# Kernel optimization log

Measured on AMD Instinct MI355X. Metric: run time of the kernel, lower is better.

## Reference

```python
import jax, jax.numpy as jnp
import numpy as np

NUM_NETS = 262144
PINS_PER_NET = 4
NUM_PINS = NUM_NETS * PINS_PER_NET
NBX, NBY = 256, 256
XL, XH, YL, YH = 0.0, 512.0, 0.0, 512.0
BSX = (XH - XL) / NBX
BSY = (YH - YL) / NBY

# RISA wiring-distribution weight table, indexed by pin count (clamped at 46).
_RISA_TAB = jnp.asarray(np.array(
    [1.0, 1.0, 1.0, 1.0,
     1.0828, 1.1536, 1.2206, 1.2823, 1.3385, 1.3991, 1.4493]
    + [1.6899] * 5 + [1.8924] * 5 + [2.0743] * 5 + [2.2334] * 5
    + [2.3892] * 5 + [2.5356] * 5 + [2.6625] * 5 + [2.7933],
    dtype=np.float32))


def setup_inputs() -> dict:
    key = jax.random.key(0)
    k1, k2 = jax.random.split(key)
    # pin positions, interleaved xyxy..., uniform inside the layout region
    pin_pos = jax.random.uniform(k1, (2 * NUM_PINS,), jnp.float32, XL, XH)
    # CSR offsets: 4 pins per net (ragged structure handled generically below)
    netpin_start = jnp.arange(NUM_NETS + 1, dtype=jnp.int32) * PINS_PER_NET
    # flat net->pin map: a permutation of all pin ids
    flat_netpin = jax.random.permutation(k2, jnp.arange(NUM_PINS, dtype=jnp.int32))
    net_weights = jnp.ones((NUM_NETS,), jnp.float32)
    return {"pin_pos": pin_pos, "netpin_start": netpin_start,
            "flat_netpin": flat_netpin, "net_weights": net_weights}


def _net_density(pin_pos, netpin_start, flat_netpin, net_weights):
    num_nets = netpin_start.shape[0] - 1
    num_pins = flat_netpin.shape[0]
    # pin i (in flat order) belongs to net n with netpin_start[n] <= i < netpin_start[n+1]
    pin2net = jnp.searchsorted(netpin_start,
                               jnp.arange(num_pins, dtype=netpin_start.dtype),
                               side='right') - 1
    px = pin_pos[2 * flat_netpin]
    py = pin_pos[2 * flat_netpin + 1]
    # per-net bounding boxes via segment max/min
    x_max = jax.ops.segment_max(px, pin2net, num_segments=num_nets)
    x_min = -jax.ops.segment_max(-px, pin2net, num_segments=num_nets)
    y_max = jax.ops.segment_max(py, pin2net, num_segments=num_nets)
    y_min = -jax.ops.segment_max(-py, pin2net, num_segments=num_nets)
    # RISA weight from pin count, times the net weight
    cnt = netpin_start[1:] - netpin_start[:-1]
    wt = _RISA_TAB[jnp.minimum(cnt, _RISA_TAB.shape[0] - 1)] * net_weights
    # per-bin overlap lengths (separable in x and y): [num_nets, NBX] / [num_nets, NBY]
    bxl = XL + BSX * jnp.arange(NBX, dtype=pin_pos.dtype)
    byl = YL + BSY * jnp.arange(NBY, dtype=pin_pos.dtype)
    ox = jnp.clip(jnp.minimum(x_max[:, None], bxl + BSX) - jnp.maximum(x_min[:, None], bxl), 0.0)
    oy = jnp.clip(jnp.minimum(y_max[:, None], byl + BSY) - jnp.maximum(y_min[:, None], byl), 0.0)
    dx = x_max - x_min
    dy = y_max - y_min
    # horizontal demand ~ wt/dy, vertical demand ~ wt/dx (guard degenerate bboxes)
    ch = jnp.where(dy > 0, wt / jnp.maximum(dy, 1e-12), 0.0)
    cv = jnp.where(dx > 0, wt / jnp.maximum(dx, 1e-12), 0.0)
    # scatter-add over bins expressed as a dense contraction over nets
    H = jnp.einsum('nx,ny->xy', ch[:, None] * ox, oy)
    V = jnp.einsum('nx,ny->xy', cv[:, None] * ox, oy)
    return jnp.abs(H) + jnp.abs(V), H, V


def reference(pin_pos, netpin_start, flat_netpin, net_weights):
    return _net_density(pin_pos, netpin_start, flat_netpin, net_weights)
```

## Files before the change

kernel.cpp:

```cpp
#include <hip/hip_runtime.h>


#define NBX 256
#define NBY 256
#define CELLS (NBX * NBY)
#define STRIPS 16
#define SROWS 16
#define HALF_TILE (SROWS * NBY)
#define TILE_FLOATS (HALF_TILE * 2)
#define NSCAT 512
#define TOTAL_ENT 724992

#define BS_ 2.0f
#define INV_BS 0.5f

__constant__ float c_risa[47] = {
    1.0f, 1.0f, 1.0f, 1.0f,
    1.0828f, 1.1536f, 1.2206f, 1.2823f, 1.3385f, 1.3991f, 1.4493f,
    1.6899f, 1.6899f, 1.6899f, 1.6899f, 1.6899f,
    1.8924f, 1.8924f, 1.8924f, 1.8924f, 1.8924f,
    2.0743f, 2.0743f, 2.0743f, 2.0743f, 2.0743f,
    2.2334f, 2.2334f, 2.2334f, 2.2334f, 2.2334f,
    2.3892f, 2.3892f, 2.3892f, 2.3892f, 2.3892f,
    2.5356f, 2.5356f, 2.5356f, 2.5356f, 2.5356f,
    2.6625f, 2.6625f, 2.6625f, 2.6625f, 2.6625f,
    2.7933f};

__constant__ int c_bcnt[STRIPS] = {58,48,39,31,25,21,18,16,
                                   16,18,21,25,31,39,48,58};
__constant__ int c_boff[STRIPS + 1] = {0,58,106,145,176,201,222,240,256,
                                       272,290,311,336,367,406,454,512};
__constant__ int c_cap[STRIPS] = {81920,67584,54272,44032,35840,29696,25600,23552,
                                  23552,25600,29696,35840,44032,54272,67584,81920};
__constant__ int c_loff[STRIPS] = {0,81920,149504,203776,247808,283648,313344,338944,
                                   362496,386048,411648,441344,477184,521216,575488,643072};

__device__ __forceinline__ unsigned enc_x(float v) {
    float r = rintf(v * 8192.0f);
    r = fminf(fmaxf(r, 0.0f), 4194303.0f);
    return (unsigned)r;
}
__device__ __forceinline__ unsigned enc_y(float v) {
    float r = rintf(v * 128.0f);
    r = fminf(fmaxf(r, 0.0f), 65535.0f);
    return (unsigned)r;
}

__global__ void zero_cursors(int* __restrict__ cursors) {
    if (threadIdx.x < STRIPS) cursors[threadIdx.x] = 0;
}

__global__ __launch_bounds__(256) void bbox_lists(
        const float* __restrict__ pin_pos,
        const int* __restrict__ netpin_start,
        const int* __restrict__ flat_netpin,
        const float* __restrict__ net_weights,
        int4* __restrict__ list, int* __restrict__ cursors, int num_nets) {
    __shared__ int cnt[STRIPS];
    __shared__ int base_[STRIPS];
    int tid = threadIdx.x;
    if (tid < STRIPS) cnt[tid] = 0;
    __syncthreads();

    int n = blockIdx.x * 256 + tid;
    int st0 = -1, st1 = -1, st2 = -1, st3 = -1;
    int p0 = 0, p1 = 0, p2 = 0, p3 = 0;
    int4 r0 = make_int4(0, 0, 0, 0), r1 = make_int4(0, 0, 0, 0);
    if (n < num_nets) {
        int s = netpin_start[n];
        int e = netpin_start[n + 1];
        int pc = e - s;
        float xmin, xmax, ymin, ymax;
        if (pc == 4 && (s & 3) == 0) {
            int4 pid = *reinterpret_cast<const int4*>(flat_netpin + s);
            float2 q0 = *reinterpret_cast<const float2*>(pin_pos + 2 * (size_t)pid.x);
            float2 q1 = *reinterpret_cast<const float2*>(pin_pos + 2 * (size_t)pid.y);
            float2 q2 = *reinterpret_cast<const float2*>(pin_pos + 2 * (size_t)pid.z);
            float2 q3 = *reinterpret_cast<const float2*>(pin_pos + 2 * (size_t)pid.w);
            xmin = fminf(fminf(q0.x, q1.x), fminf(q2.x, q3.x));
            xmax = fmaxf(fmaxf(q0.x, q1.x), fmaxf(q2.x, q3.x));
            ymin = fminf(fminf(q0.y, q1.y), fminf(q2.y, q3.y));
            ymax = fmaxf(fmaxf(q0.y, q1.y), fmaxf(q2.y, q3.y));
        } else {
            xmin = 1e30f; xmax = -1e30f; ymin = 1e30f; ymax = -1e30f;
            for (int i = s; i < e; ++i) {
                int p = flat_netpin[i];
                float2 xy = *reinterpret_cast<const float2*>(pin_pos + 2 * (long)p);
                xmin = fminf(xmin, xy.x);
                xmax = fmaxf(xmax, xy.x);
                ymin = fminf(ymin, xy.y);
                ymax = fmaxf(ymax, xy.y);
            }
        }
        if (pc > 0) {
            float wt = c_risa[min(pc, 46)] * net_weights[n];
            float dx = xmax - xmin;
            float dy = ymax - ymin;
            float ch = (dy > 0.0f) ? wt / fmaxf(dy, 1e-12f) : 0.0f;
            float cv = (dx > 0.0f) ? wt / fmaxf(dx, 1e-12f) : 0.0f;
            if (ch != 0.0f || cv != 0.0f) {
                unsigned xf1 = enc_x(xmin), xf2 = enc_x(xmax);
                unsigned ypk = enc_y(ymin) | (enc_y(ymax) << 16);
                r0 = make_int4((int)xf1, (int)ypk, __float_as_int(ch), __float_as_int(cv));
                r1 = make_int4((int)xf2, (int)ypk, __float_as_int(-ch), __float_as_int(-cv));
                int k1 = xf1 >> 14;
                int k2 = xf2 >> 14;
                if (k1 < 256) {
                    st0 = k1 >> 4;
                    p0 = atomicAdd(&cnt[st0], 1);
                    int kb = k1 + 1;
                    if (kb < 256 && (kb >> 4) != st0) { st1 = kb >> 4; p1 = atomicAdd(&cnt[st1], 1); }
                }
                if (k2 < 256) {
                    st2 = k2 >> 4;
                    p2 = atomicAdd(&cnt[st2], 1);
                    int kb = k2 + 1;
                    if (kb < 256 && (kb >> 4) != st2) { st3 = kb >> 4; p3 = atomicAdd(&cnt[st3], 1); }
                }
            }
        }
    }
    __syncthreads();
    if (tid < STRIPS) base_[tid] = cnt[tid] ? atomicAdd(&cursors[tid], cnt[tid]) : 0;
    __syncthreads();
    if (st0 >= 0) { int pos = base_[st0] + p0; if (pos < c_cap[st0]) list[c_loff[st0] + pos] = r0; }
    if (st1 >= 0) { int pos = base_[st1] + p1; if (pos < c_cap[st1]) list[c_loff[st1] + pos] = r0; }
    if (st2 >= 0) { int pos = base_[st2] + p2; if (pos < c_cap[st2]) list[c_loff[st2] + pos] = r1; }
    if (st3 >= 0) { int pos = base_[st3] + p3; if (pos < c_cap[st3]) list[c_loff[st3] + pos] = r1; }
}

__global__ __launch_bounds__(512) void strip_scatter(
        const int4* __restrict__ list, const int* __restrict__ cursors,
        float* __restrict__ P) {
    __shared__ float lds[TILE_FLOATS];
    int bid = blockIdx.x;
    int strip = 0;
#pragma unroll
    for (int s = 1; s < STRIPS; ++s)
        if (bid >= c_boff[s]) strip = s;
    int sub = bid - c_boff[strip];
    int nb = c_bcnt[strip];
    int lo = strip * SROWS;
    int tid = threadIdx.x;
    float4* z = (float4*)lds;
    for (int j = tid; j < TILE_FLOATS / 4; j += 512) z[j] = make_float4(0, 0, 0, 0);
    __syncthreads();

    int len = min(cursors[strip], c_cap[strip]);
    const int4* A = list + c_loff[strip];
    int chunk = (len + nb - 1) / nb;
    int i0 = sub * chunk;
    int i1 = min(i0 + chunk, len);
    for (int i = i0 + tid; i < i1; i += 512) {
        int4 a = A[i];
        unsigned xf = (unsigned)a.x;
        int k = xf >> 14;
        float f = (float)(xf & 16383) * (1.0f / 16384.0f);
        int ks = (int)((xf + 8192u) >> 14);
        unsigned yp = (unsigned)a.y;
        unsigned y1 = yp & 0xffffu, y2 = yp >> 16;
        int j1 = (int)(y1 >> 8);
        float g1 = (float)(y1 & 255u) * (1.0f / 256.0f);
        int j2 = (int)(y2 >> 8);
        float g2 = (float)(y2 & 255u) * (1.0f / 256.0f);
        int js1 = (int)((y1 + 128u) >> 8);
        int js2 = (int)((y2 + 128u) >> 8);
        float sch = __int_as_float(a.z);
        float scv = __int_as_float(a.w);

        int rh = ks - lo;
        if ((unsigned)rh < SROWS) {
            float w = sch * (BS_ * BS_);
            int rbase = rh * NBY;
            if (j1 < NBY)     unsafeAtomicAdd(&lds[rbase + j1],      w * (1.0f - g1));
            if (j1 + 1 < NBY) unsafeAtomicAdd(&lds[rbase + j1 + 1],  w * g1);
            if (j2 < NBY)     unsafeAtomicAdd(&lds[rbase + j2],     -w * (1.0f - g2));
            if (j2 + 1 < NBY) unsafeAtomicAdd(&lds[rbase + j2 + 1], -w * g2);
        }
        if (js1 != js2) {
            float wv = scv * (BS_ * BS_);
            float w0 = wv * (1.0f - f);
            float w1 = wv * f;
#pragma unroll
            for (int r = 0; r < 2; ++r) {
                int rr = k + r - lo;
                if ((unsigned)rr >= SROWS) continue;
                float w = r ? w1 : w0;
                int rbase = HALF_TILE + rr * NBY;
                if (js1 < NBY) unsafeAtomicAdd(&lds[rbase + js1],  w);
                if (js2 < NBY) unsafeAtomicAdd(&lds[rbase + js2], -w);
            }
        }
    }
    __syncthreads();
    float4* dst = (float4*)(P + (size_t)bid * TILE_FLOATS);
    const float4* src = (const float4*)lds;
    for (int j = tid; j < TILE_FLOATS / 4; j += 512) dst[j] = src[j];
}

__global__ void merge_scany(const float* __restrict__ P, float2* __restrict__ T) {
    __shared__ float sh[256];
    __shared__ float sv[256];
    int x = blockIdx.x;
    int t = threadIdx.x;
    int strip = x >> 4;
    int r = x & 15;
    int b0 = c_boff[strip], b1 = c_boff[strip + 1];
    const float* base = P + (size_t)b0 * TILE_FLOATS + r * NBY + t;
    float h = 0.0f, v = 0.0f;
    for (int b = b0; b < b1; ++b) {
        h += base[0];
        v += base[HALF_TILE];
        base += TILE_FLOATS;
    }
    sh[t] = h; sv[t] = v;
    __syncthreads();
    for (int off = 1; off < 256; off <<= 1) {
        float ah = (t >= off) ? sh[t - off] : 0.0f;
        float av = (t >= off) ? sv[t - off] : 0.0f;
        __syncthreads();
        sh[t] += ah;
        sv[t] += av;
        __syncthreads();
    }
    T[x * NBY + t] = make_float2(sh[t], sv[t]);
}

__global__ void scanx_out(const float2* __restrict__ T, float* __restrict__ out) {
    __shared__ float sh[256];
    __shared__ float sv[256];
    int y = blockIdx.x;
    int t = threadIdx.x;
    float2 c = T[t * NBY + y];
    sh[t] = c.x; sv[t] = c.y;
    __syncthreads();
    for (int off = 1; off < 256; off <<= 1) {
        float ah = (t >= off) ? sh[t - off] : 0.0f;
        float av = (t >= off) ? sv[t - off] : 0.0f;
        __syncthreads();
        sh[t] += ah;
        sv[t] += av;
        __syncthreads();
    }
    float h = sh[t], v = sv[t];
    int idx = t * NBY + y;
    out[idx] = fabsf(h) + fabsf(v);
    out[CELLS + idx] = h;
    out[2 * CELLS + idx] = v;
}

__global__ void zero_dense(float* __restrict__ S) {
    int i = blockIdx.x * blockDim.x + threadIdx.x;
    if (i < CELLS * 2) S[i] = 0.0f;
}

__global__ void fused_atomic(const float* __restrict__ pin_pos,
                             const int* __restrict__ netpin_start,
                             const int* __restrict__ flat_netpin,
                             const float* __restrict__ net_weights,
                             float* __restrict__ S, int num_nets) {
    int n = blockIdx.x * blockDim.x + threadIdx.x;
    if (n >= num_nets) return;
    int s = netpin_start[n];
    int e = netpin_start[n + 1];
    int pc = e - s;
    if (pc <= 0) return;
    float xmin = 1e30f, xmax = -1e30f, ymin = 1e30f, ymax = -1e30f;
    for (int i = s; i < e; ++i) {
        int p = flat_netpin[i];
        float2 xy = *reinterpret_cast<const float2*>(pin_pos + 2 * (long)p);
        xmin = fminf(xmin, xy.x);
        xmax = fmaxf(xmax, xy.x);
        ymin = fminf(ymin, xy.y);
        ymax = fmaxf(ymax, xy.y);
    }
    float wt = c_risa[min(pc, 46)] * net_weights[n];
    float dx = xmax - xmin;
    float dy = ymax - ymin;
    float ch = (dy > 0.0f) ? wt / fmaxf(dy, 1e-12f) : 0.0f;
    float cv = (dx > 0.0f) ? wt / fmaxf(dx, 1e-12f) : 0.0f;
    if (ch == 0.0f && cv == 0.0f) return;
    float t1 = xmin * INV_BS, t2 = xmax * INV_BS;
    int k1 = min(max((int)floorf(t1), 0), 256);
    int k2 = min(max((int)floorf(t2), 0), 256);
    float fx1 = t1 - k1, fx2 = t2 - k2;
    float u1 = ymin * INV_BS, u2 = ymax * INV_BS;
    int j1 = min(max((int)floorf(u1), 0), 256);
    int j2 = min(max((int)floorf(u2), 0), 256);
    float fy1 = u1 - j1, fy2 = u2 - j2;
    int   xi[4] = {k1, k1 + 1, k2, k2 + 1};
    float xw[4] = {BS_ * (1 - fx1), BS_ * fx1, -BS_ * (1 - fx2), -BS_ * fx2};
    int   yi[4] = {j1, j1 + 1, j2, j2 + 1};
    float yw[4] = {BS_ * (1 - fy1), BS_ * fy1, -BS_ * (1 - fy2), -BS_ * fy2};
#pragma unroll
    for (int a = 0; a < 4; ++a) {
        if (xi[a] >= NBX) continue;
        int rbase = xi[a] * NBY;
        float wh = ch * xw[a];
        float wv = cv * xw[a];
#pragma unroll
        for (int b = 0; b < 4; ++b) {
            if (yi[b] >= NBY) continue;
            int off = rbase + yi[b];
            atomicAdd(&S[off], wh * yw[b]);
            atomicAdd(&S[off + CELLS], wv * yw[b]);
        }
    }
}

__global__ void scany_dense(const float* __restrict__ S, float2* __restrict__ T) {
    __shared__ float sh[256];
    __shared__ float sv[256];
    int x = blockIdx.x;
    int t = threadIdx.x;
    sh[t] = S[x * NBY + t];
    sv[t] = S[CELLS + x * NBY + t];
    __syncthreads();
    for (int off = 1; off < 256; off <<= 1) {
        float ah = (t >= off) ? sh[t - off] : 0.0f;
        float av = (t >= off) ? sv[t - off] : 0.0f;
        __syncthreads();
        sh[t] += ah;
        sv[t] += av;
        __syncthreads();
    }
    T[x * NBY + t] = make_float2(sh[t], sv[t]);
}

static inline size_t alignup(size_t v, size_t a) { return (v + a - 1) & ~(a - 1); }

extern "C" void kernel_launch(void* const* d_in, const int* in_sizes, int n_in,
                              void* d_out, int out_size, void* d_ws, size_t ws_size,
                              hipStream_t stream) {
    const float* pin_pos = (const float*)d_in[0];
    const int* netpin_start = (const int*)d_in[1];
    const int* flat_netpin = (const int*)d_in[2];
    const float* net_weights = (const float*)d_in[3];
    int num_nets = in_sizes[1] - 1;

    size_t off = 0;
    size_t list_off = off; off = alignup(off + (size_t)TOTAL_ENT * 16, 16);
    size_t P_off = off;    off = alignup(off + (size_t)NSCAT * TILE_FLOATS * 4, 16);
    size_t T_off = off;    off = alignup(off + (size_t)CELLS * 8, 16);
    size_t cur_off = off;  off += 256;
    size_t need = off;

    float* out = (float*)d_out;
    char* ws = (char*)d_ws;
    int nb = (num_nets + 255) / 256;

    if (ws_size >= need && num_nets <= 262144) {
        int4* list = (int4*)(ws + list_off);
        float* P = (float*)(ws + P_off);
        float2* T = (float2*)(ws + T_off);
        int* cursors = (int*)(ws + cur_off);
        zero_cursors<<<1, 64, 0, stream>>>(cursors);
        bbox_lists<<<nb, 256, 0, stream>>>(pin_pos, netpin_start, flat_netpin,
                                           net_weights, list, cursors, num_nets);
        strip_scatter<<<NSCAT, 512, 0, stream>>>(list, cursors, P);
        merge_scany<<<NBX, 256, 0, stream>>>(P, T);
        scanx_out<<<NBY, 256, 0, stream>>>(T, out);
    } else {
        float* S = (float*)ws;
        float2* T = (float2*)(ws + (size_t)CELLS * 2 * sizeof(float));
        zero_dense<<<(CELLS * 2 + 255) / 256, 256, 0, stream>>>(S);
        fused_atomic<<<nb, 256, 0, stream>>>(pin_pos, netpin_start, flat_netpin,
                                             net_weights, S, num_nets);
        scany_dense<<<NBX, 256, 0, stream>>>(S, T);
        scanx_out<<<NBY, 256, 0, stream>>>(T, out);
    }
}
```

Baseline: 84.37 us.

## Pre-pack pin coordinates to 16-bit fixed point before bbox gather

Adds a pack_pins pass that quantizes each pin's x/y to 16-bit fixed point (1/128 units) in one 32-bit word, so the random gather in bbox_lists reads 4 bytes per pin instead of 8. It also zeroes the cursors inside that pass, removing the separate zero_cursors launch. Bbox min/max become integer ops, and the x encoding drops from 1/8192 to 1/128 resolution, with strip_scatter decoding to match. The cost is an extra streaming pass over pin_pos, and dx/dy and the bin fractions are now computed from quantized coordinates, which loses accuracy.

```diff
diff --git a/kernel.cpp b/kernel.cpp
--- a/kernel.cpp
+++ b/kernel.cpp
@@ -35,23 +35,21 @@
 __constant__ int c_loff[STRIPS] = {0,81920,149504,203776,247808,283648,313344,338944,
                                    362496,386048,411648,441344,477184,521216,575488,643072};
 
-__device__ __forceinline__ unsigned enc_x(float v) {
-    float r = rintf(v * 8192.0f);
-    r = fminf(fmaxf(r, 0.0f), 4194303.0f);
-    return (unsigned)r;
-}
-__device__ __forceinline__ unsigned enc_y(float v) {
-    float r = rintf(v * 128.0f);
-    r = fminf(fmaxf(r, 0.0f), 65535.0f);
-    return (unsigned)r;
-}
-
-__global__ void zero_cursors(int* __restrict__ cursors) {
-    if (threadIdx.x < STRIPS) cursors[threadIdx.x] = 0;
+
+__global__ __launch_bounds__(256) void pack_pins(
+        const float* __restrict__ pin_pos, unsigned* __restrict__ ppack,
+        int* __restrict__ cursors, int num_pins) {
+    int i = blockIdx.x * 256 + threadIdx.x;
+    if (blockIdx.x == 0 && threadIdx.x < STRIPS) cursors[threadIdx.x] = 0;
+    if (i >= num_pins) return;
+    float2 xy = *reinterpret_cast<const float2*>(pin_pos + 2 * (size_t)i);
+    float xr = fminf(fmaxf(rintf(xy.x * 128.0f), 0.0f), 65535.0f);
+    float yr = fminf(fmaxf(rintf(xy.y * 128.0f), 0.0f), 65535.0f);
+    ppack[i] = (unsigned)xr | ((unsigned)yr << 16);
 }
 
 __global__ __launch_bounds__(256) void bbox_lists(
-        const float* __restrict__ pin_pos,
+        const unsigned* __restrict__ ppack,
         const int* __restrict__ netpin_start,
         const int* __restrict__ flat_netpin,
         const float* __restrict__ net_weights,
@@ -70,48 +68,48 @@
         int s = netpin_start[n];
         int e = netpin_start[n + 1];
         int pc = e - s;
-        float xmin, xmax, ymin, ymax;
+        unsigned xmin = 65535u, xmax = 0u, ymin = 65535u, ymax = 0u;
         if (pc == 4 && (s & 3) == 0) {
             int4 pid = *reinterpret_cast<const int4*>(flat_netpin + s);
-            float2 q0 = *reinterpret_cast<const float2*>(pin_pos + 2 * (size_t)pid.x);
-            float2 q1 = *reinterpret_cast<const float2*>(pin_pos + 2 * (size_t)pid.y);
-            float2 q2 = *reinterpret_cast<const float2*>(pin_pos + 2 * (size_t)pid.z);
-            float2 q3 = *reinterpret_cast<const float2*>(pin_pos + 2 * (size_t)pid.w);
-            xmin = fminf(fminf(q0.x, q1.x), fminf(q2.x, q3.x));
-            xmax = fmaxf(fmaxf(q0.x, q1.x), fmaxf(q2.x, q3.x));
-            ymin = fminf(fminf(q0.y, q1.y), fminf(q2.y, q3.y));
-            ymax = fmaxf(fmaxf(q0.y, q1.y), fmaxf(q2.y, q3.y));
+            unsigned q0 = ppack[pid.x];
+            unsigned q1 = ppack[pid.y];
+            unsigned q2 = ppack[pid.z];
+            unsigned q3 = ppack[pid.w];
+            unsigned x0 = q0 & 0xffffu, x1 = q1 & 0xffffu;
+            unsigned x2 = q2 & 0xffffu, x3 = q3 & 0xffffu;
+            unsigned v0 = q0 >> 16, v1 = q1 >> 16, v2 = q2 >> 16, v3 = q3 >> 16;
+            xmin = min(min(x0, x1), min(x2, x3));
+            xmax = max(max(x0, x1), max(x2, x3));
+            ymin = min(min(v0, v1), min(v2, v3));
+            ymax = max(max(v0, v1), max(v2, v3));
         } else {
-            xmin = 1e30f; xmax = -1e30f; ymin = 1e30f; ymax = -1e30f;
             for (int i = s; i < e; ++i) {
                 int p = flat_netpin[i];
-                float2 xy = *reinterpret_cast<const float2*>(pin_pos + 2 * (long)p);
-                xmin = fminf(xmin, xy.x);
-                xmax = fmaxf(xmax, xy.x);
-                ymin = fminf(ymin, xy.y);
-                ymax = fmaxf(ymax, xy.y);
+                unsigned q = ppack[p];
+                unsigned x = q & 0xffffu, y = q >> 16;
+                xmin = min(xmin, x); xmax = max(xmax, x);
+                ymin = min(ymin, y); ymax = max(ymax, y);
             }
         }
         if (pc > 0) {
             float wt = c_risa[min(pc, 46)] * net_weights[n];
-            float dx = xmax - xmin;
-            float dy = ymax - ymin;
+            float dx = (float)(xmax - xmin) * (1.0f / 128.0f);
+            float dy = (float)(ymax - ymin) * (1.0f / 128.0f);
             float ch = (dy > 0.0f) ? wt / fmaxf(dy, 1e-12f) : 0.0f;
             float cv = (dx > 0.0f) ? wt / fmaxf(dx, 1e-12f) : 0.0f;
             if (ch != 0.0f || cv != 0.0f) {
-                unsigned xf1 = enc_x(xmin), xf2 = enc_x(xmax);
-                unsigned ypk = enc_y(ymin) | (enc_y(ymax) << 16);
-                r0 = make_int4((int)xf1, (int)ypk, __float_as_int(ch), __float_as_int(cv));
-                r1 = make_int4((int)xf2, (int)ypk, __float_as_int(-ch), __float_as_int(-cv));
-                int k1 = xf1 >> 14;
-                int k2 = xf2 >> 14;
-                if (k1 < 256) {
+                unsigned ypk = ymin | (ymax << 16);
+                r0 = make_int4((int)xmin, (int)ypk, __float_as_int(ch), __float_as_int(cv));
+                r1 = make_int4((int)xmax, (int)ypk, __float_as_int(-ch), __float_as_int(-cv));
+                int k1 = xmin >> 8;
+                int k2 = xmax >> 8;
+                {
                     st0 = k1 >> 4;
                     p0 = atomicAdd(&cnt[st0], 1);
                     int kb = k1 + 1;
                     if (kb < 256 && (kb >> 4) != st0) { st1 = kb >> 4; p1 = atomicAdd(&cnt[st1], 1); }
                 }
-                if (k2 < 256) {
+                {
                     st2 = k2 >> 4;
                     p2 = atomicAdd(&cnt[st2], 1);
                     int kb = k2 + 1;
@@ -154,9 +152,9 @@
     for (int i = i0 + tid; i < i1; i += 512) {
         int4 a = A[i];
         unsigned xf = (unsigned)a.x;
-        int k = xf >> 14;
-        float f = (float)(xf & 16383) * (1.0f / 16384.0f);
-        int ks = (int)((xf + 8192u) >> 14);
+        int k = xf >> 8;
+        float f = (float)(xf & 255u) * (1.0f / 256.0f);
+        int ks = (int)((xf + 128u) >> 8);
         unsigned yp = (unsigned)a.y;
         unsigned y1 = yp & 0xffffu, y2 = yp >> 16;
         int j1 = (int)(y1 >> 8);
@@ -337,8 +335,10 @@
     const int* flat_netpin = (const int*)d_in[2];
     const float* net_weights = (const float*)d_in[3];
     int num_nets = in_sizes[1] - 1;
+    int num_pins = in_sizes[2];
 
     size_t off = 0;
+    size_t pk_off = off;   off = alignup(off + (size_t)num_pins * 4, 16);
     size_t list_off = off; off = alignup(off + (size_t)TOTAL_ENT * 16, 16);
     size_t P_off = off;    off = alignup(off + (size_t)NSCAT * TILE_FLOATS * 4, 16);
     size_t T_off = off;    off = alignup(off + (size_t)CELLS * 8, 16);
@@ -350,12 +350,14 @@
     int nb = (num_nets + 255) / 256;
 
     if (ws_size >= need && num_nets <= 262144) {
+        unsigned* ppack = (unsigned*)(ws + pk_off);
         int4* list = (int4*)(ws + list_off);
         float* P = (float*)(ws + P_off);
         float2* T = (float2*)(ws + T_off);
         int* cursors = (int*)(ws + cur_off);
-        zero_cursors<<<1, 64, 0, stream>>>(cursors);
-        bbox_lists<<<nb, 256, 0, stream>>>(pin_pos, netpin_start, flat_netpin,
+        pack_pins<<<(num_pins + 255) / 256, 256, 0, stream>>>(pin_pos, ppack,
+                                                              cursors, num_pins);
+        bbox_lists<<<nb, 256, 0, stream>>>(ppack, netpin_start, flat_netpin,
                                            net_weights, list, cursors, num_nets);
         strip_scatter<<<NSCAT, 512, 0, stream>>>(list, cursors, P);
         merge_scany<<<NBX, 256, 0, stream>>>(P, T);
```

Result: faster. 81.37 us (-3.5%).
